# Optimization experiments

Measured on AMD Instinct MI355X. Metric: run time of the kernel, lower is better.

The kernel has to match this reference:

```python
import jax, jax.numpy as jnp
import numpy as np

GROUP = 32          # microscale group size for both acts and weights
FP8_MAX = 448.0     # float8_e4m3fn max
FP4_TABLE = jnp.array([0.0, 0.5, 1.0, 1.5, 2.0, 3.0, 4.0, 6.0,
                       -0.0, -0.5, -1.0, -1.5, -2.0, -3.0, -4.0, -6.0], dtype=jnp.float32)


def _ue8m0_to_float(sf):
    # uint8 exponent byte placed directly into the fp32 exponent field: 2^(e-127)
    return jax.lax.bitcast_convert_type(sf.astype(jnp.uint32) << 23, jnp.float32)


def _dequant_mxfp4(w_packed, sf):
    # w_packed: [..., K//2] ints in [0,256), two e2m1 nibbles per byte (low nibble = even elem)
    lo = FP4_TABLE[w_packed & 0xF]
    hi = FP4_TABLE[(w_packed >> 4) & 0xF]
    w = jnp.stack([lo, hi], axis=-1).reshape(*w_packed.shape[:-1], -1)   # [..., K]
    s = _ue8m0_to_float(sf)                                              # [..., K//32]
    w = w.reshape(*sf.shape, GROUP) * s[..., None]
    return w.reshape(*w_packed.shape[:-1], 2 * w_packed.shape[-1])


def _quant_dequant_fp8(x):
    # Faithful to _deepseek_v4_stage_mega_moe_inputs_kernel: per-32-group amax,
    # scale = amax/448 rounded UP to a power of two (UE8M0), cast to fp8 e4m3.
    T, D = x.shape
    xg = x.reshape(T, D // GROUP, GROUP)
    amax = jnp.maximum(jnp.max(jnp.abs(xg), axis=-1), 1e-4)
    scale = amax / FP8_MAX
    bits = jax.lax.bitcast_convert_type(scale, jnp.uint32)
    exp = ((bits >> 23) & 0xFF) + ((bits & 0x7FFFFF) != 0).astype(jnp.uint32)
    exp = jnp.clip(exp, 1, 254)
    rscale = jax.lax.bitcast_convert_type(exp << 23, jnp.float32)
    q = (xg * (1.0 / rscale)[..., None]).astype(jnp.float8_e4m3fn)
    return (q.astype(jnp.float32) * rscale[..., None]).reshape(T, D)


def setup_inputs() -> dict:
    key = jax.random.key(0)
    ks = jax.random.split(key, 7)
    T, D, I, E, K = 512, 2048, 768, 16, 8
    hidden_states = jax.random.normal(ks[0], (T, D), dtype=jnp.float32)
    topk_weights = jax.random.uniform(ks[1], (T, K), dtype=jnp.float32)
    topk_weights = topk_weights / jnp.sum(topk_weights, axis=-1, keepdims=True)
    topk_ids = jax.random.randint(ks[2], (T, K), 0, E, dtype=jnp.int32)
    w13_weight = jax.random.randint(ks[3], (E, 2 * I, D // 2), 0, 256, dtype=jnp.int32)
    w13_weight_scale = jax.random.randint(ks[4], (E, 2 * I, D // GROUP), 120, 128, dtype=jnp.int32)
    w2_weight = jax.random.randint(ks[5], (E, D, I // 2), 0, 256, dtype=jnp.int32)
    w2_weight_scale = jax.random.randint(ks[6], (E, D, I // GROUP), 120, 128, dtype=jnp.int32)
    return {"hidden_states": hidden_states, "topk_weights": topk_weights,
            "topk_ids": topk_ids, "w13_weight": w13_weight,
            "w13_weight_scale": w13_weight_scale, "w2_weight": w2_weight,
            "w2_weight_scale": w2_weight_scale}


def reference(hidden_states, topk_weights, topk_ids, w13_weight, w13_weight_scale,
              w2_weight, w2_weight_scale):
    E = w13_weight.shape[0]
    I = w13_weight.shape[1] // 2
    x = _quant_dequant_fp8(hidden_states)                 # [T, D] fp8-quantized acts
    w13 = _dequant_mxfp4(w13_weight, w13_weight_scale)    # [E, 2I, D]
    w2 = _dequant_mxfp4(w2_weight, w2_weight_scale)       # [E, D, I]
    onehot = (topk_ids[:, :, None] == jnp.arange(E)[None, None, :]).astype(jnp.float32)  # [T,K,E]
    routed = jnp.any(onehot > 0, axis=1)                  # [T, E]
    Xe = routed.T[:, :, None].astype(x.dtype) * x[None]   # [E, T, D]
    h = jnp.einsum('etd,efd->etf', Xe, w13)               # [E, T, 2I]
    gate, up = h[..., :I], h[..., I:]
    a = jax.nn.silu(gate) * up                            # SiluAndMul
    ye = jnp.einsum('eti,edi->etd', a, w2)                # [E, T, D]
    comb = jnp.einsum('tke,tk->te', onehot, topk_weights) # [T, E] routing weights
    return jnp.einsum('te,etd->td', comb, ye)             # [T, D]
```

## Files before the change

kernel.cpp:

```cpp
#include <hip/hip_runtime.h>
#include <stdint.h>
#include <math.h>

#define T_TOK 512
#define DDIM  2048
#define IDIM  768
#define NEXP  16
#define TOPK  8
#define LDA   72

typedef __attribute__((ext_vector_type(8))) short bf16x8;
typedef __attribute__((ext_vector_type(4))) float f32x4;

__device__ __forceinline__ float e4m3_rtne(float f) {
  uint32_t u = __float_as_uint(f);
  uint32_t sign = u & 0x80000000u;
  uint32_t a = u & 0x7FFFFFFFu;
  float fa = __uint_as_float(a);
  float out;
  if (fa >= 0.015625f) {
    uint32_t lsb = (a >> 20) & 1u;
    a += 0x0007FFFFu + lsb;
    a &= 0xFFF00000u;
    out = __uint_as_float(a);
  } else {
    out = rintf(fa * 512.0f) * 0.001953125f;
  }
  return __uint_as_float(__float_as_uint(out) | sign);
}

__global__ void qdq_kernel(const float* __restrict__ x, ushort* __restrict__ xq) {
  int idx = blockIdx.x * 256 + threadIdx.x;
  float v = x[idx];
  float a = fabsf(v);
#pragma unroll
  for (int m = 16; m >= 1; m >>= 1)
    a = fmaxf(a, __shfl_xor(a, m, 32));
  a = fmaxf(a, 1e-4f);
  float scale = a / 448.0f;
  uint32_t b = __float_as_uint(scale);
  uint32_t ex = ((b >> 23) & 255u) + ((b & 0x7FFFFFu) ? 1u : 0u);
  ex = ex < 1u ? 1u : (ex > 254u ? 254u : ex);
  float rscale = __uint_as_float(ex << 23);
  float inv = 1.0f / rscale;
  float r = e4m3_rtne(v * inv) * rscale;
  xq[idx] = (ushort)(__float_as_uint(r) >> 16);
}

__global__ void route_kernel(const int* __restrict__ ids, const float* __restrict__ wts,
                             int* counts, int* offsets, int* lists, float* combs,
                             int* tpe, int* tps, int* tpn) {
  int t = threadIdx.x;
  int  myid[TOPK];
  float myw[TOPK];
#pragma unroll
  for (int k = 0; k < TOPK; k++) { myid[k] = ids[t*TOPK+k]; myw[k] = wts[t*TOPK+k]; }
  int np = 0;
  for (int e = 0; e < NEXP; e++) {
    float s = 0.f; bool r = false;
#pragma unroll
    for (int k = 0; k < TOPK; k++) if (myid[k] == e) { s += myw[k]; r = true; }
    if (r) {
      int slot = atomicAdd(&counts[e], 1);
      lists[(e<<9) + slot] = t;
      combs[(e<<9) + slot] = s;
      tpe[t*TOPK + np] = e;
      tps[t*TOPK + np] = slot;
      np++;
    }
  }
  tpn[t] = np;
  __syncthreads();
  if (t == 0) {
    int acc = 0;
    for (int e = 0; e < NEXP; e++) {
      offsets[e] = acc;
      acc += atomicAdd(&counts[e], 0);
    }
    offsets[NEXP] = acc;
  }
}

__device__ __forceinline__ uint32_t dec2(uint32_t w8, uint32_t S) {
  uint32_t lo = w8 & 15u, hi = (w8 >> 4) & 15u;
  uint32_t mlo = lo & 7u, mhi = hi & 7u;
  uint32_t clo = (mlo < 2u) ? 0u : mlo;
  uint32_t chi = (mhi < 2u) ? 0u : mhi;
  uint32_t blo = (mlo == 0u) ? 0u : ((S + clo) << 6);
  uint32_t bhi = (mhi == 0u) ? 0u : ((S + chi) << 6);
  blo |= (lo & 8u) << 12;
  bhi |= (hi & 8u) << 12;
  return blo | (bhi << 16);
}

__global__ __launch_bounds__(256,2) void gemm1_kernel(
    const ushort* __restrict__ xq, const int* __restrict__ w13,
    const int* __restrict__ w13s, const int* __restrict__ counts,
    const int* __restrict__ offsets, const int* __restrict__ lists,
    const float* __restrict__ combs, ushort* __restrict__ a_buf)
{
  const int e  = blockIdx.x;
  const int i0 = blockIdx.y << 6;
  const int m0 = blockIdx.z << 8;
  const int cnt = counts[e];
  if (m0 >= cnt) return;

  __shared__ __align__(16) ushort As[256*LDA];
  __shared__ __align__(16) ushort Bg[64*LDA];
  __shared__ __align__(16) ushort Bu[64*LDA];
  __shared__ int   toks[256];
  __shared__ float cmbs[256];

  const int tid = threadIdx.x;
  {
    int m = m0 + tid;
    bool v = m < cnt;
    toks[tid] = v ? lists[(e<<9)+m] : -1;
    cmbs[tid] = v ? combs[(e<<9)+m] : 0.f;
  }
  __syncthreads();

  const int ar = tid >> 2;
  const int ac = (tid & 3) << 4;
  int atok[4];
#pragma unroll
  for (int p = 0; p < 4; p++) atok[p] = toks[ar + (p<<6)];

  const int br = tid >> 1;
  const int bh = tid & 1;
  const int bfeat = (br < 64) ? (i0 + br) : (IDIM + i0 + (br - 64));
  const int* wrow = w13 + ((size_t)(e * 2 * IDIM) + bfeat) * (DDIM/2);
  const int* srow = w13s + ((size_t)(e * 2 * IDIM) + bfeat) * (DDIM/32);
  ushort* Brow = ((br < 64) ? Bg : Bu) + (br & 63) * LDA + (bh << 5);

  const int lane = tid & 63;
  const int wv = tid >> 6;
  const int l16 = lane & 15;
  const int q   = lane >> 4;

  f32x4 accg[4][4] = {{{0,0,0,0}}}, accu[4][4] = {{{0,0,0,0}}};

  for (int k0 = 0; k0 < DDIM; k0 += 64) {
    int4 av[4][2];
#pragma unroll
    for (int p = 0; p < 4; p++) {
      if (atok[p] >= 0) {
        const int4* src = (const int4*)(xq + (size_t)atok[p]*DDIM + k0 + ac);
        av[p][0] = src[0]; av[p][1] = src[1];
      } else {
        av[p][0] = make_int4(0,0,0,0); av[p][1] = make_int4(0,0,0,0);
      }
    }
    const int4* bp = (const int4*)(wrow + (k0 >> 1)) + (bh << 2);
    int4 wv0 = bp[0], wv1 = bp[1], wv2 = bp[2], wv3 = bp[3];
    uint32_t S = (((uint32_t)srow[(k0 >> 5) + bh]) - 1u) << 1;

    __syncthreads();
#pragma unroll
    for (int p = 0; p < 4; p++) {
      *(int4*)&As[(ar + (p<<6))*LDA + ac]     = av[p][0];
      *(int4*)&As[(ar + (p<<6))*LDA + ac + 8] = av[p][1];
    }
    {
      int wq[16] = {wv0.x,wv0.y,wv0.z,wv0.w, wv1.x,wv1.y,wv1.z,wv1.w,
                    wv2.x,wv2.y,wv2.z,wv2.w, wv3.x,wv3.y,wv3.z,wv3.w};
      uint32_t o[16];
#pragma unroll
      for (int j = 0; j < 16; j++) o[j] = dec2((uint32_t)wq[j], S);
#pragma unroll
      for (int c = 0; c < 4; c++)
        *(int4*)&Brow[c*8] = make_int4((int)o[4*c], (int)o[4*c+1], (int)o[4*c+2], (int)o[4*c+3]);
    }
    __syncthreads();

#pragma unroll
    for (int s = 0; s < 2; s++) {
      bf16x8 af[4];
#pragma unroll
      for (int i = 0; i < 4; i++)
        af[i] = *(const bf16x8*)&As[(wv*64 + i*16 + l16)*LDA + s*32 + q*8];
#pragma unroll
      for (int j = 0; j < 4; j++) {
        bf16x8 bg = *(const bf16x8*)&Bg[(j*16 + l16)*LDA + s*32 + q*8];
        bf16x8 bu = *(const bf16x8*)&Bu[(j*16 + l16)*LDA + s*32 + q*8];
#pragma unroll
        for (int i = 0; i < 4; i++) {
          accg[i][j] = __builtin_amdgcn_mfma_f32_16x16x32_bf16(af[i], bg, accg[i][j], 0, 0, 0);
          accu[i][j] = __builtin_amdgcn_mfma_f32_16x16x32_bf16(af[i], bu, accu[i][j], 0, 0, 0);
        }
      }
    }
  }

  const int obase = offsets[e];
#pragma unroll
  for (int i = 0; i < 4; i++) {
#pragma unroll
    for (int r = 0; r < 4; r++) {
      int mrow = wv*64 + i*16 + q*4 + r;
      int gm = m0 + mrow;
      if (gm < cnt) {
        float c = cmbs[mrow];
        ushort* dst = a_buf + (size_t)(obase + gm)*IDIM + i0 + l16;
#pragma unroll
        for (int j = 0; j < 4; j++) {
          float g = accg[i][j][r], u = accu[i][j][r];
          float val = (g / (1.f + expf(-g))) * u * c;
          uint32_t bb = __float_as_uint(val);
          bb += 0x7FFFu + ((bb >> 16) & 1u);
          dst[j*16] = (ushort)(bb >> 16);
        }
      }
    }
  }
}

__global__ __launch_bounds__(256,2) void gemm2_kernel(
    const ushort* __restrict__ a_buf, const int* __restrict__ w2,
    const int* __restrict__ w2s, const int* __restrict__ counts,
    const int* __restrict__ offsets, const int* __restrict__ lists,
    float* __restrict__ out, float* __restrict__ ye, int use_ye)
{
  const int e  = blockIdx.x;
  const int n0 = blockIdx.y << 6;
  const int m0 = blockIdx.z << 8;
  const int cnt = counts[e];
  if (m0 >= cnt) return;

  __shared__ __align__(16) ushort As[256*LDA];
  __shared__ __align__(16) ushort Bs[64*LDA];
  __shared__ int toks[256];

  const int tid = threadIdx.x;
  {
    int m = m0 + tid;
    toks[tid] = (m < cnt) ? lists[(e<<9)+m] : -1;
  }
  __syncthreads();

  const int obase = offsets[e];
  const int ar = tid >> 2;
  const int ac = (tid & 3) << 4;

  const int br = tid >> 2;
  const int bq = tid & 3;
  const int* wrow = w2 + ((size_t)(e * DDIM) + n0 + br) * (IDIM/2);
  const int* srow = w2s + ((size_t)(e * DDIM) + n0 + br) * (IDIM/32);
  ushort* Brow = Bs + br * LDA + (bq << 4);

  const int lane = tid & 63;
  const int wv = tid >> 6;
  const int l16 = lane & 15;
  const int q   = lane >> 4;

  f32x4 acc[4][4] = {{{0,0,0,0}}};

  for (int k0 = 0; k0 < IDIM; k0 += 64) {
    int4 av[4][2];
#pragma unroll
    for (int p = 0; p < 4; p++) {
      int gm = m0 + ar + (p<<6);
      if (gm < cnt) {
        const int4* src = (const int4*)(a_buf + (size_t)(obase + gm)*IDIM + k0 + ac);
        av[p][0] = src[0]; av[p][1] = src[1];
      } else {
        av[p][0] = make_int4(0,0,0,0); av[p][1] = make_int4(0,0,0,0);
      }
    }
    const int4* bp = (const int4*)(wrow + (k0 >> 1)) + (bq << 1);
    int4 wv0 = bp[0], wv1 = bp[1];
    uint32_t S = (((uint32_t)srow[(k0 >> 5) + (bq >> 1)]) - 1u) << 1;

    __syncthreads();
#pragma unroll
    for (int p = 0; p < 4; p++) {
      *(int4*)&As[(ar + (p<<6))*LDA + ac]     = av[p][0];
      *(int4*)&As[(ar + (p<<6))*LDA + ac + 8] = av[p][1];
    }
    {
      int wq[8] = {wv0.x,wv0.y,wv0.z,wv0.w, wv1.x,wv1.y,wv1.z,wv1.w};
      uint32_t o[8];
#pragma unroll
      for (int j = 0; j < 8; j++) o[j] = dec2((uint32_t)wq[j], S);
      *(int4*)&Brow[0] = make_int4((int)o[0], (int)o[1], (int)o[2], (int)o[3]);
      *(int4*)&Brow[8] = make_int4((int)o[4], (int)o[5], (int)o[6], (int)o[7]);
    }
    __syncthreads();

#pragma unroll
    for (int s = 0; s < 2; s++) {
      bf16x8 af[4];
#pragma unroll
      for (int i = 0; i < 4; i++)
        af[i] = *(const bf16x8*)&As[(wv*64 + i*16 + l16)*LDA + s*32 + q*8];
#pragma unroll
      for (int j = 0; j < 4; j++) {
        bf16x8 bb = *(const bf16x8*)&Bs[(j*16 + l16)*LDA + s*32 + q*8];
#pragma unroll
        for (int i = 0; i < 4; i++)
          acc[i][j] = __builtin_amdgcn_mfma_f32_16x16x32_bf16(af[i], bb, acc[i][j], 0, 0, 0);
      }
    }
  }

#pragma unroll
  for (int i = 0; i < 4; i++) {
#pragma unroll
    for (int r = 0; r < 4; r++) {
      int mrow = wv*64 + i*16 + q*4 + r;
      int gm = m0 + mrow;
      if (gm < cnt) {
        if (use_ye) {
          float* dst = ye + (size_t)(obase + gm)*DDIM + n0 + l16;
#pragma unroll
          for (int j = 0; j < 4; j++) dst[j*16] = acc[i][j][r];
        } else {
          int tok = toks[mrow];
          float* dst = out + (size_t)tok*DDIM + n0 + l16;
#pragma unroll
          for (int j = 0; j < 4; j++) atomicAdd(&dst[j*16], acc[i][j][r]);
        }
      }
    }
  }
}

__global__ void combine_kernel(const float* __restrict__ ye, const int* __restrict__ offsets,
                               const int* __restrict__ tpe, const int* __restrict__ tps,
                               const int* __restrict__ tpn, float* __restrict__ out) {
  int t = blockIdx.x;
  int np = tpn[t];
  int rows[TOPK];
#pragma unroll
  for (int j = 0; j < TOPK; j++)
    rows[j] = (j < np) ? (offsets[tpe[t*TOPK+j]] + tps[t*TOPK+j]) : -1;
  for (int c = threadIdx.x; c < DDIM; c += 256) {
    float s = 0.f;
#pragma unroll
    for (int j = 0; j < TOPK; j++)
      if (rows[j] >= 0) s += ye[(size_t)rows[j]*DDIM + c];
    out[(size_t)t*DDIM + c] = s;
  }
}

extern "C" void kernel_launch(void* const* d_in, const int* in_sizes, int n_in,
                              void* d_out, int out_size, void* d_ws, size_t ws_size,
                              hipStream_t stream)
{
  const float* x    = (const float*)d_in[0];
  const float* tw   = (const float*)d_in[1];
  const int*   tids = (const int*)d_in[2];
  const int*   w13  = (const int*)d_in[3];
  const int*   w13s = (const int*)d_in[4];
  const int*   w2   = (const int*)d_in[5];
  const int*   w2s  = (const int*)d_in[6];
  float* out = (float*)d_out;

  char* ws = (char*)d_ws;
  size_t off = 0;
  ushort* xq     = (ushort*)(ws + off);  off += (size_t)T_TOK*DDIM*2;
  int*   counts  = (int*)(ws + off);     off += 256;
  int*   offsets = (int*)(ws + off);     off += 256;
  int*   lists   = (int*)(ws + off);     off += (size_t)NEXP*T_TOK*4;
  float* combs   = (float*)(ws + off);   off += (size_t)NEXP*T_TOK*4;
  int*   tpe     = (int*)(ws + off);     off += (size_t)T_TOK*TOPK*4;
  int*   tps     = (int*)(ws + off);     off += (size_t)T_TOK*TOPK*4;
  int*   tpn     = (int*)(ws + off);     off += (size_t)T_TOK*4;
  ushort* a_buf  = (ushort*)(ws + off);  off += (size_t)T_TOK*TOPK*IDIM*2;
  float* ye      = (float*)(ws + off);
  size_t need_ye = off + (size_t)T_TOK*TOPK*DDIM*4;
  int use_ye = (ws_size >= need_ye) ? 1 : 0;

  hipMemsetAsync(counts, 0, 256, stream);
  hipMemsetAsync(out, 0, (size_t)out_size * 4, stream);

  qdq_kernel<<<(T_TOK*DDIM)/256, 256, 0, stream>>>(x, xq);
  route_kernel<<<1, T_TOK, 0, stream>>>(tids, tw, counts, offsets, lists, combs, tpe, tps, tpn);
  gemm1_kernel<<<dim3(NEXP, IDIM/64, 2), 256, 0, stream>>>(
      xq, w13, w13s, counts, offsets, lists, combs, a_buf);
  gemm2_kernel<<<dim3(NEXP, DDIM/64, 2), 256, 0, stream>>>(
      a_buf, w2, w2s, counts, offsets, lists, out, ye, use_ye);
  if (use_ye)
    combine_kernel<<<T_TOK, 256, 0, stream>>>(ye, offsets, tpe, tps, tpn, out);
}
```

Measured before the change: 322.4 us.

## Shrink GEMM tiles and load activation fragments directly from global memory

Both expert GEMMs now use 128-thread blocks with 128-row M tiles (and 32-wide gate/up feature tiles in gemm1). Activation MFMA fragments are read straight from global memory into registers instead of being staged through shared memory, so only the dequantized weight tile lives in LDS. The grid gets more blocks to spread work across CUs and LDS use drops, at the cost of uncoalesced per-lane activation reads and less reuse of each decoded weight tile. The workspace allocator also pads each buffer to 256-byte alignment.

Result: slower. 335.5 us (+4.1%).

```diff
diff --git a/kernel.cpp b/kernel.cpp
--- a/kernel.cpp
+++ b/kernel.cpp
@@ -7,7 +7,7 @@
 #define IDIM  768
 #define NEXP  16
 #define TOPK  8
-#define LDA   72
+#define LDB   72
 
 typedef __attribute__((ext_vector_type(8))) short bf16x8;
 typedef __attribute__((ext_vector_type(4))) float f32x4;
@@ -93,102 +93,86 @@
   return blo | (bhi << 16);
 }
 
-__global__ __launch_bounds__(256,2) void gemm1_kernel(
+__global__ __launch_bounds__(128,2) void gemm1_kernel(
     const ushort* __restrict__ xq, const int* __restrict__ w13,
     const int* __restrict__ w13s, const int* __restrict__ counts,
     const int* __restrict__ offsets, const int* __restrict__ lists,
     const float* __restrict__ combs, ushort* __restrict__ a_buf)
 {
   const int e  = blockIdx.x;
-  const int i0 = blockIdx.y << 6;
-  const int m0 = blockIdx.z << 8;
+  const int i0 = blockIdx.y << 5;
+  const int m0 = blockIdx.z << 7;
   const int cnt = counts[e];
   if (m0 >= cnt) return;
 
-  __shared__ __align__(16) ushort As[256*LDA];
-  __shared__ __align__(16) ushort Bg[64*LDA];
-  __shared__ __align__(16) ushort Bu[64*LDA];
-  __shared__ int   toks[256];
-  __shared__ float cmbs[256];
+  __shared__ __align__(16) ushort Bsh[64*LDB];
+  __shared__ int   toks[128];
+  __shared__ float cmbs[128];
 
   const int tid = threadIdx.x;
-  {
-    int m = m0 + tid;
-    bool v = m < cnt;
-    toks[tid] = v ? lists[(e<<9)+m] : -1;
-    cmbs[tid] = v ? combs[(e<<9)+m] : 0.f;
-  }
+  { int m = m0 + tid; bool v = m < cnt;
+    toks[tid] = v ? lists[(e<<9)+m] : 0;
+    cmbs[tid] = v ? combs[(e<<9)+m] : 0.f; }
   __syncthreads();
 
-  const int ar = tid >> 2;
-  const int ac = (tid & 3) << 4;
-  int atok[4];
-#pragma unroll
-  for (int p = 0; p < 4; p++) atok[p] = toks[ar + (p<<6)];
-
-  const int br = tid >> 1;
-  const int bh = tid & 1;
-  const int bfeat = (br < 64) ? (i0 + br) : (IDIM + i0 + (br - 64));
-  const int* wrow = w13 + ((size_t)(e * 2 * IDIM) + bfeat) * (DDIM/2);
-  const int* srow = w13s + ((size_t)(e * 2 * IDIM) + bfeat) * (DDIM/32);
-  ushort* Brow = ((br < 64) ? Bg : Bu) + (br & 63) * LDA + (bh << 5);
-
-  const int lane = tid & 63;
-  const int wv = tid >> 6;
-  const int l16 = lane & 15;
-  const int q   = lane >> 4;
-
-  f32x4 accg[4][4] = {{{0,0,0,0}}}, accu[4][4] = {{{0,0,0,0}}};
+  const int wv = tid >> 6, l = tid & 63, l16 = l & 15, q = l >> 4;
+
+  const ushort* arow[4];
+#pragma unroll
+  for (int i = 0; i < 4; i++) {
+    int row = wv*64 + i*16 + l16;
+    arow[i] = xq + (size_t)toks[row]*DDIM + q*8;
+  }
+
+  const int rb = tid >> 1, hb = tid & 1;
+  const int feat = (rb < 32) ? (i0 + rb) : (IDIM + i0 + (rb - 32));
+  const int* wrow = w13 + ((size_t)e*(2*IDIM) + feat)*(DDIM/2) + hb*16;
+  const int* srow = w13s + ((size_t)e*(2*IDIM) + feat)*(DDIM/32);
+  ushort* bdst = Bsh + rb*LDB + hb*32;
+
+  f32x4 acc[4][4];
+#pragma unroll
+  for (int i = 0; i < 4; i++)
+#pragma unroll
+    for (int j = 0; j < 4; j++) acc[i][j] = (f32x4){0.f,0.f,0.f,0.f};
 
   for (int k0 = 0; k0 < DDIM; k0 += 64) {
-    int4 av[4][2];
-#pragma unroll
-    for (int p = 0; p < 4; p++) {
-      if (atok[p] >= 0) {
-        const int4* src = (const int4*)(xq + (size_t)atok[p]*DDIM + k0 + ac);
-        av[p][0] = src[0]; av[p][1] = src[1];
-      } else {
-        av[p][0] = make_int4(0,0,0,0); av[p][1] = make_int4(0,0,0,0);
-      }
-    }
-    const int4* bp = (const int4*)(wrow + (k0 >> 1)) + (bh << 2);
-    int4 wv0 = bp[0], wv1 = bp[1], wv2 = bp[2], wv3 = bp[3];
-    uint32_t S = (((uint32_t)srow[(k0 >> 5) + bh]) - 1u) << 1;
+    int4 wq[4];
+    const int4* bp = (const int4*)(wrow + (k0 >> 1));
+#pragma unroll
+    for (int c = 0; c < 4; c++) wq[c] = bp[c];
+    uint32_t S = (((uint32_t)srow[(k0 >> 5) + hb]) - 1u) << 1;
+
+    bf16x8 afr[4][2];
+#pragma unroll
+    for (int i = 0; i < 4; i++)
+#pragma unroll
+      for (int s = 0; s < 2; s++)
+        afr[i][s] = *(const bf16x8*)(arow[i] + k0 + s*32);
 
     __syncthreads();
-#pragma unroll
-    for (int p = 0; p < 4; p++) {
-      *(int4*)&As[(ar + (p<<6))*LDA + ac]     = av[p][0];
-      *(int4*)&As[(ar + (p<<6))*LDA + ac + 8] = av[p][1];
-    }
     {
-      int wq[16] = {wv0.x,wv0.y,wv0.z,wv0.w, wv1.x,wv1.y,wv1.z,wv1.w,
-                    wv2.x,wv2.y,wv2.z,wv2.w, wv3.x,wv3.y,wv3.z,wv3.w};
-      uint32_t o[16];
-#pragma unroll
-      for (int j = 0; j < 16; j++) o[j] = dec2((uint32_t)wq[j], S);
+      uint32_t od[16];
+      const int* wi = (const int*)wq;
+#pragma unroll
+      for (int c = 0; c < 16; c++) od[c] = dec2((uint32_t)wi[c], S);
 #pragma unroll
       for (int c = 0; c < 4; c++)
-        *(int4*)&Brow[c*8] = make_int4((int)o[4*c], (int)o[4*c+1], (int)o[4*c+2], (int)o[4*c+3]);
+        *(uint4*)(bdst + c*8) = make_uint4(od[4*c], od[4*c+1], od[4*c+2], od[4*c+3]);
     }
     __syncthreads();
 
 #pragma unroll
     for (int s = 0; s < 2; s++) {
-      bf16x8 af[4];
+      bf16x8 bfr[4];
+#pragma unroll
+      for (int j = 0; j < 4; j++)
+        bfr[j] = *(const bf16x8*)(Bsh + (j*16 + l16)*LDB + s*32 + q*8);
 #pragma unroll
       for (int i = 0; i < 4; i++)
-        af[i] = *(const bf16x8*)&As[(wv*64 + i*16 + l16)*LDA + s*32 + q*8];
-#pragma unroll
-      for (int j = 0; j < 4; j++) {
-        bf16x8 bg = *(const bf16x8*)&Bg[(j*16 + l16)*LDA + s*32 + q*8];
-        bf16x8 bu = *(const bf16x8*)&Bu[(j*16 + l16)*LDA + s*32 + q*8];
-#pragma unroll
-        for (int i = 0; i < 4; i++) {
-          accg[i][j] = __builtin_amdgcn_mfma_f32_16x16x32_bf16(af[i], bg, accg[i][j], 0, 0, 0);
-          accu[i][j] = __builtin_amdgcn_mfma_f32_16x16x32_bf16(af[i], bu, accu[i][j], 0, 0, 0);
-        }
-      }
+#pragma unroll
+        for (int j = 0; j < 4; j++)
+          acc[i][j] = __builtin_amdgcn_mfma_f32_16x16x32_bf16(afr[i][s], bfr[j], acc[i][j], 0, 0, 0);
     }
   }
 
@@ -203,19 +187,19 @@
         float c = cmbs[mrow];
         ushort* dst = a_buf + (size_t)(obase + gm)*IDIM + i0 + l16;
 #pragma unroll
-        for (int j = 0; j < 4; j++) {
-          float g = accg[i][j][r], u = accu[i][j][r];
+        for (int jj = 0; jj < 2; jj++) {
+          float g = acc[i][jj][r], u = acc[i][jj+2][r];
           float val = (g / (1.f + expf(-g))) * u * c;
           uint32_t bb = __float_as_uint(val);
           bb += 0x7FFFu + ((bb >> 16) & 1u);
-          dst[j*16] = (ushort)(bb >> 16);
+          dst[jj*16] = (ushort)(bb >> 16);
         }
       }
     }
   }
 }
 
-__global__ __launch_bounds__(256,2) void gemm2_kernel(
+__global__ __launch_bounds__(128,2) void gemm2_kernel(
     const ushort* __restrict__ a_buf, const int* __restrict__ w2,
     const int* __restrict__ w2s, const int* __restrict__ counts,
     const int* __restrict__ offsets, const int* __restrict__ lists,
@@ -223,83 +207,76 @@
 {
   const int e  = blockIdx.x;
   const int n0 = blockIdx.y << 6;
-  const int m0 = blockIdx.z << 8;
+  const int m0 = blockIdx.z << 7;
   const int cnt = counts[e];
   if (m0 >= cnt) return;
 
-  __shared__ __align__(16) ushort As[256*LDA];
-  __shared__ __align__(16) ushort Bs[64*LDA];
-  __shared__ int toks[256];
+  __shared__ __align__(16) ushort Bsh[64*LDB];
+  __shared__ int toks[128];
 
   const int tid = threadIdx.x;
-  {
-    int m = m0 + tid;
-    toks[tid] = (m < cnt) ? lists[(e<<9)+m] : -1;
-  }
+  { int m = m0 + tid; toks[tid] = (m < cnt) ? lists[(e<<9)+m] : -1; }
   __syncthreads();
 
+  const int wv = tid >> 6, l = tid & 63, l16 = l & 15, q = l >> 4;
   const int obase = offsets[e];
-  const int ar = tid >> 2;
-  const int ac = (tid & 3) << 4;
-
-  const int br = tid >> 2;
-  const int bq = tid & 3;
-  const int* wrow = w2 + ((size_t)(e * DDIM) + n0 + br) * (IDIM/2);
-  const int* srow = w2s + ((size_t)(e * DDIM) + n0 + br) * (IDIM/32);
-  ushort* Brow = Bs + br * LDA + (bq << 4);
-
-  const int lane = tid & 63;
-  const int wv = tid >> 6;
-  const int l16 = lane & 15;
-  const int q   = lane >> 4;
-
-  f32x4 acc[4][4] = {{{0,0,0,0}}};
+
+  const ushort* arow[4];
+#pragma unroll
+  for (int i = 0; i < 4; i++) {
+    int gm = m0 + wv*64 + i*16 + l16;
+    int rowc = (gm < cnt) ? gm : 0;
+    arow[i] = a_buf + (size_t)(obase + rowc)*IDIM + q*8;
+  }
+
+  const int rb = tid >> 1, hb = tid & 1;
+  const int* wrow = w2 + ((size_t)e*DDIM + n0 + rb)*(IDIM/2) + hb*16;
+  const int* srow = w2s + ((size_t)e*DDIM + n0 + rb)*(IDIM/32);
+  ushort* bdst = Bsh + rb*LDB + hb*32;
+
+  f32x4 acc[4][4];
+#pragma unroll
+  for (int i = 0; i < 4; i++)
+#pragma unroll
+    for (int j = 0; j < 4; j++) acc[i][j] = (f32x4){0.f,0.f,0.f,0.f};
 
   for (int k0 = 0; k0 < IDIM; k0 += 64) {
-    int4 av[4][2];
-#pragma unroll
-    for (int p = 0; p < 4; p++) {
-      int gm = m0 + ar + (p<<6);
-      if (gm < cnt) {
-        const int4* src = (const int4*)(a_buf + (size_t)(obase + gm)*IDIM + k0 + ac);
-        av[p][0] = src[0]; av[p][1] = src[1];
-      } else {
-        av[p][0] = make_int4(0,0,0,0); av[p][1] = make_int4(0,0,0,0);
-      }
-    }
-    const int4* bp = (const int4*)(wrow + (k0 >> 1)) + (bq << 1);
-    int4 wv0 = bp[0], wv1 = bp[1];
-    uint32_t S = (((uint32_t)srow[(k0 >> 5) + (bq >> 1)]) - 1u) << 1;
+    int4 wq[4];
+    const int4* bp = (const int4*)(wrow + (k0 >> 1));
+#pragma unroll
+    for (int c = 0; c < 4; c++) wq[c] = bp[c];
+    uint32_t S = (((uint32_t)srow[(k0 >> 5) + hb]) - 1u) << 1;
+
+    bf16x8 afr[4][2];
+#pragma unroll
+    for (int i = 0; i < 4; i++)
+#pragma unroll
+      for (int s = 0; s < 2; s++)
+        afr[i][s] = *(const bf16x8*)(arow[i] + k0 + s*32);
 
     __syncthreads();
-#pragma unroll
-    for (int p = 0; p < 4; p++) {
-      *(int4*)&As[(ar + (p<<6))*LDA + ac]     = av[p][0];
-      *(int4*)&As[(ar + (p<<6))*LDA + ac + 8] = av[p][1];
-    }
     {
-      int wq[8] = {wv0.x,wv0.y,wv0.z,wv0.w, wv1.x,wv1.y,wv1.z,wv1.w};
-      uint32_t o[8];
-#pragma unroll
-      for (int j = 0; j < 8; j++) o[j] = dec2((uint32_t)wq[j], S);
-      *(int4*)&Brow[0] = make_int4((int)o[0], (int)o[1], (int)o[2], (int)o[3]);
-      *(int4*)&Brow[8] = make_int4((int)o[4], (int)o[5], (int)o[6], (int)o[7]);
+      uint32_t od[16];
+      const int* wi = (const int*)wq;
+#pragma unroll
+      for (int c = 0; c < 16; c++) od[c] = dec2((uint32_t)wi[c], S);
+#pragma unroll
+      for (int c = 0; c < 4; c++)
+        *(uint4*)(bdst + c*8) = make_uint4(od[4*c], od[4*c+1], od[4*c+2], od[4*c+3]);
     }
     __syncthreads();
 
 #pragma unroll
     for (int s = 0; s < 2; s++) {
-      bf16x8 af[4];
+      bf16x8 bfr[4];
+#pragma unroll
+      for (int j = 0; j < 4; j++)
+        bfr[j] = *(const bf16x8*)(Bsh + (j*16 + l16)*LDB + s*32 + q*8);
 #pragma unroll
       for (int i = 0; i < 4; i++)
-        af[i] = *(const bf16x8*)&As[(wv*64 + i*16 + l16)*LDA + s*32 + q*8];
-#pragma unroll
-      for (int j = 0; j < 4; j++) {
-        bf16x8 bb = *(const bf16x8*)&Bs[(j*16 + l16)*LDA + s*32 + q*8];
-#pragma unroll
-        for (int i = 0; i < 4; i++)
-          acc[i][j] = __builtin_amdgcn_mfma_f32_16x16x32_bf16(af[i], bb, acc[i][j], 0, 0, 0);
-      }
+#pragma unroll
+        for (int j = 0; j < 4; j++)
+          acc[i][j] = __builtin_amdgcn_mfma_f32_16x16x32_bf16(afr[i][s], bfr[j], acc[i][j], 0, 0, 0);
     }
   }
 
@@ -358,15 +335,16 @@
 
   char* ws = (char*)d_ws;
   size_t off = 0;
-  ushort* xq     = (ushort*)(ws + off);  off += (size_t)T_TOK*DDIM*2;
-  int*   counts  = (int*)(ws + off);     off += 256;
-  int*   offsets = (int*)(ws + off);     off += 256;
-  int*   lists   = (int*)(ws + off);     off += (size_t)NEXP*T_TOK*4;
-  float* combs   = (float*)(ws + off);   off += (size_t)NEXP*T_TOK*4;
-  int*   tpe     = (int*)(ws + off);     off += (size_t)T_TOK*TOPK*4;
-  int*   tps     = (int*)(ws + off);     off += (size_t)T_TOK*TOPK*4;
-  int*   tpn     = (int*)(ws + off);     off += (size_t)T_TOK*4;
-  ushort* a_buf  = (ushort*)(ws + off);  off += (size_t)T_TOK*TOPK*IDIM*2;
+  auto alloc = [&](size_t bytes) { void* p = ws + off; off = (off + bytes + 255) & ~(size_t)255; return p; };
+  ushort* xq     = (ushort*)alloc((size_t)T_TOK*DDIM*2);
+  int*   counts  = (int*)alloc(64*4);
+  int*   offsets = (int*)alloc(64*4);
+  int*   lists   = (int*)alloc((size_t)NEXP*T_TOK*4);
+  float* combs   = (float*)alloc((size_t)NEXP*T_TOK*4);
+  int*   tpe     = (int*)alloc((size_t)T_TOK*TOPK*4);
+  int*   tps     = (int*)alloc((size_t)T_TOK*TOPK*4);
+  int*   tpn     = (int*)alloc((size_t)T_TOK*4);
+  ushort* a_buf  = (ushort*)alloc((size_t)T_TOK*TOPK*IDIM*2);
   float* ye      = (float*)(ws + off);
   size_t need_ye = off + (size_t)T_TOK*TOPK*DDIM*4;
   int use_ye = (ws_size >= need_ye) ? 1 : 0;
@@ -376,9 +354,9 @@
 
   qdq_kernel<<<(T_TOK*DDIM)/256, 256, 0, stream>>>(x, xq);
   route_kernel<<<1, T_TOK, 0, stream>>>(tids, tw, counts, offsets, lists, combs, tpe, tps, tpn);
-  gemm1_kernel<<<dim3(NEXP, IDIM/64, 2), 256, 0, stream>>>(
+  gemm1_kernel<<<dim3(NEXP, IDIM/32, 4), 128, 0, stream>>>(
       xq, w13, w13s, counts, offsets, lists, combs, a_buf);
-  gemm2_kernel<<<dim3(NEXP, DDIM/64, 2), 256, 0, stream>>>(
+  gemm2_kernel<<<dim3(NEXP, DDIM/64, 4), 128, 0, stream>>>(
       a_buf, w2, w2s, counts, offsets, lists, out, ye, use_ye);
   if (use_ye)
     combine_kernel<<<T_TOK, 256, 0, stream>>>(ye, offsets, tpe, tps, tpn, out);
```
